# Optimization experiments

Hardware: AMD Instinct MI355X
Metric: run time of the kernel (lower is better)

Reference implementation:

```python
import jax, jax.numpy as jnp
import numpy as np

B, K, NP = 2, 48, 25            # batch, context_length, grid_x*grid_y
C, H, L = 768, 12, 6            # n_embd, n_head, n_layer
COLORS, VOCAB, IS = 10, 40, 26  # color_num, vocab_size, intention_size
MAXT = 1000                     # max_timestep
TOK = NP + 4                    # tokens per timestep (rtg, 25 states, action, pnp, intention)
T = K * TOK                     # total sequence length


def layernorm(x, g, b, eps=1e-5):
    m = x.mean(-1, keepdims=True)
    v = ((x - m) ** 2).mean(-1, keepdims=True)
    return (x - m) * jax.lax.rsqrt(v + eps) * g + b


def causal_attn(x, wq, bq, wk, bk, wv, bv, wo, bo):
    Bx, Tx, Cx = x.shape
    hd = Cx // H
    def heads(w, bb):
        return (x @ w + bb).reshape(Bx, Tx, H, hd).transpose(0, 2, 1, 3)
    q, k, v = heads(wq, bq), heads(wk, bk), heads(wv, bv)
    att = jnp.einsum('bhqd,bhkd->bhqk', q, k) * (1.0 / np.sqrt(hd))
    mask = jnp.tril(jnp.ones((Tx, Tx), bool))
    att = jnp.where(mask, att, -jnp.inf)
    att = jax.nn.softmax(att, axis=-1)
    y = jnp.einsum('bhqk,bhkd->bhqd', att, v).transpose(0, 2, 1, 3).reshape(Bx, Tx, Cx)
    return y @ wo + bo


def setup_inputs() -> dict:
    key = jax.random.key(0)
    ks = iter(jax.random.split(key, 64))
    def nrm(shape):
        return jax.random.normal(next(ks), shape, jnp.float32) * 0.02
    inp = dict(
        states=jax.random.randint(next(ks), (B, K * NP), 0, COLORS),
        actions=jax.random.randint(next(ks), (B, K), 0, VOCAB),
        rtgs=jax.random.normal(next(ks), (B, K), jnp.float32),
        timesteps=jax.random.randint(next(ks), (B, K), 0, MAXT + 1),
        pnp=jax.random.normal(next(ks), (B, K, NP), jnp.float32),
        intentions=jax.random.randint(next(ks), (B, K, 2), 0, IS),
        pos_emb=nrm((K + 1, C)),               # (block_size, C)
        global_pos_emb=nrm((MAXT + 1, C)),
        state_tab=nrm((COLORS, C)),
        action_tab=nrm((VOCAB, C)),
        ret_W=nrm((1, C)), ret_b=jnp.zeros((C,)),
        pnp_W=nrm((NP, C)), pnp_b=jnp.zeros((C,)),
        src_tab=nrm((IS, C)), dst_tab=nrm((IS, C)),
        int_W=nrm((2 * C, C)), int_b=jnp.zeros((C,)),
        ln1_g=jnp.ones((L, C)), ln1_b=jnp.zeros((L, C)),
        ln2_g=jnp.ones((L, C)), ln2_b=jnp.zeros((L, C)),
        Wq=nrm((L, C, C)), bq=jnp.zeros((L, C)),
        Wk=nrm((L, C, C)), bk=jnp.zeros((L, C)),
        Wv=nrm((L, C, C)), bv=jnp.zeros((L, C)),
        Wo=nrm((L, C, C)), bo=jnp.zeros((L, C)),
        Wm1=nrm((L, C, 4 * C)), bm1=jnp.zeros((L, 4 * C)),
        Wm2=nrm((L, 4 * C, C)), bm2=jnp.zeros((L, C)),
        lnf_g=jnp.ones((C,)), lnf_b=jnp.zeros((C,)),
        Whs=nrm((C, COLORS)), bhs=jnp.zeros((COLORS,)),
        Wha=nrm((C, VOCAB)), bha=jnp.zeros((VOCAB,)),
        Whr=nrm((C, 1)), bhr=jnp.zeros((1,)),
        Whi=nrm((C, 2 * IS)), bhi=jnp.zeros((2 * IS,)),
    )
    return inp


def reference(states, actions, rtgs, timesteps, pnp, intentions,
              pos_emb, global_pos_emb, state_tab, action_tab,
              ret_W, ret_b, pnp_W, pnp_b, src_tab, dst_tab, int_W, int_b,
              ln1_g, ln1_b, ln2_g, ln2_b, Wq, bq, Wk, bk, Wv, bv, Wo, bo,
              Wm1, bm1, Wm2, bm2, lnf_g, lnf_b,
              Whs, bhs, Wha, bha, Whr, bhr, Whi, bhi):
    # --- embeddings, interleaved as [rtg, state_0..24, action, pnp, intention] per timestep ---
    st = state_tab[states].reshape(B, K, NP, C)                    # strided writes 1+i::TOK
    ae = action_tab[actions][:, :, None, :]
    re = (rtgs[..., None] @ ret_W + ret_b)[:, :, None, :]          # rtgs.unsqueeze(-1) -> Linear(1,C)
    pe = (pnp @ pnp_W + pnp_b)[:, :, None, :]
    ie_in = jnp.concatenate([src_tab[intentions[..., 0]], dst_tab[intentions[..., 1]]], axis=-1)
    ie = (ie_in @ int_W + int_b)[:, :, None, :]
    tok = jnp.concatenate([re, st, ae, pe, ie], axis=2).reshape(B, T, C)
    # --- positions: gather global + local pos_emb[:block_size-1], repeat_interleave by TOK ---
    pos = global_pos_emb[timesteps] + pos_emb[:K][None]            # (B, K, C)
    x = tok + jnp.repeat(pos, TOK, axis=1)
    # --- transformer stack (dropout p=0) ---
    def blk(h, p):
        l1g, l1b, l2g, l2b, wq, bq_, wk, bk_, wv, bv_, wo, bo_, w1, b1, w2, b2 = p
        h = h + causal_attn(layernorm(h, l1g, l1b), wq, bq_, wk, bk_, wv, bv_, wo, bo_)
        m = layernorm(h, l2g, l2b)
        h = h + jax.nn.gelu(m @ w1 + b1, approximate=False) @ w2 + b2
        return h, None
    x, _ = jax.lax.scan(blk, x, (ln1_g, ln1_b, ln2_g, ln2_b, Wq, bq, Wk, bk, Wv, bv, Wo, bo, Wm1, bm1, Wm2, bm2))
    x = layernorm(x, lnf_g, lnf_b)
    xr = x.reshape(B, K, TOK, C)
    logits = x @ Whs + bhs                                         # (B, T, COLORS)
    logit_action = xr[:, :, NP + 1] @ Wha + bha                    # (B, K, VOCAB)
    logit_rtg = (xr[:, :, 0] @ Whr + bhr)[..., 0]                  # (B, K)
    li = xr[:, :, NP + 3] @ Whi + bhi                              # (B, K, 2*IS)
    return logits, logit_action, logit_rtg, li[..., :IS], li[..., IS:]
```

## Files before the change

kernel.cpp:

```cpp
#include <hip/hip_runtime.h>
#include <hip/hip_bf16.h>
#include <math.h>


typedef __hip_bfloat16 bf16;
typedef __attribute__((ext_vector_type(4))) short s4v;
typedef __attribute__((ext_vector_type(8))) short s8v;
typedef __attribute__((ext_vector_type(4))) float f4v;
typedef unsigned int u32;

#define DEV static __device__ __forceinline__

constexpr int NBATCH = 2;
constexpr int NK   = 48;
constexpr int NNP  = 25;
constexpr int NC   = 768;
constexpr int NH   = 12;
constexpr int NL   = 6;
constexpr int NTOK = 29;
constexpr int NT   = NK * NTOK;
constexpr int NM   = NBATCH * NT;
constexpr int MPAD = 2816;

DEV float bs2f(short s) {
  unsigned u = ((unsigned)(unsigned short)s) << 16;
  float f; __builtin_memcpy(&f, &u, 4); return f;
}
DEV short f2bs(float f) {
  bf16 h = __float2bfloat16(f);
  short s; __builtin_memcpy(&s, &h, 2); return s;
}

DEV void async16(const short* g, short* l) {
  __builtin_amdgcn_global_load_lds(
      (const __attribute__((address_space(1))) u32*)g,
      (__attribute__((address_space(3))) u32*)l, 16, 0, 0);
}

__global__ __launch_bounds__(256) void transpose_kernel(
    const float* __restrict__ src, bf16* __restrict__ dst, int R, int C)
{
  int c0 = blockIdx.x * 32, r0 = blockIdx.y * 32;
  __shared__ float tl[32][33];
  int rr = threadIdx.x >> 5, cc = threadIdx.x & 31;
#pragma unroll
  for (int p = 0; p < 4; p++)
    tl[rr + p * 8][cc] = src[(long)(r0 + rr + p * 8) * C + c0 + cc];
  __syncthreads();
#pragma unroll
  for (int p = 0; p < 4; p++)
    dst[(long)(c0 + rr + p * 8) * R + r0 + cc] = __float2bfloat16(tl[cc][rr + p * 8]);
}

__global__ __launch_bounds__(256) void transpose_layer_kernel(
    const float* __restrict__ Wq, const float* __restrict__ Wk,
    const float* __restrict__ Wv, const float* __restrict__ Wo,
    const float* __restrict__ Wm1, const float* __restrict__ Wm2,
    bf16* __restrict__ WqkvT, bf16* __restrict__ WoT,
    bf16* __restrict__ Wm1T, bf16* __restrict__ Wm2T, int multi)
{
  int blk = blockIdx.x;
  int l = blk / 1728, t = blk - l * 1728;
  long so = (long)l * 768 * 768;
  long mo = (long)l * 768 * 3072;
  long dl = multi ? l : 0;
  const float* src; bf16* dst; int R, C, tile;
  if (t < 432) {
    int m = t / 144; tile = t - m * 144;
    src = (m == 0 ? Wq : (m == 1 ? Wk : Wv)) + so;
    dst = WqkvT + dl * (2304L * 768) + (long)m * 768 * 768; R = 768; C = 768;
  } else if (t < 576)  { src = Wo + so;  dst = WoT  + dl * (768L * 768);  tile = t - 432;  R = 768;  C = 768;  }
  else if (t < 1152)   { src = Wm1 + mo; dst = Wm1T + dl * (3072L * 768); tile = t - 576;  R = 768;  C = 3072; }
  else                 { src = Wm2 + mo; dst = Wm2T + dl * (768L * 3072); tile = t - 1152; R = 3072; C = 768;  }
  int ct = C / 64;
  int tr = tile / ct, tc = tile - tr * ct;
  int r0 = tr * 64, c0 = tc * 64;

  __shared__ short tl[64][66];
  int t4 = threadIdx.x & 15, rr = threadIdx.x >> 4;
#pragma unroll
  for (int p = 0; p < 4; p++) {
    int row = rr + p * 16;
    f4v v = *(const f4v*)(src + (long)(r0 + row) * C + c0 + t4 * 4);
    tl[t4 * 4 + 0][row] = f2bs(v.x);
    tl[t4 * 4 + 1][row] = f2bs(v.y);
    tl[t4 * 4 + 2][row] = f2bs(v.z);
    tl[t4 * 4 + 3][row] = f2bs(v.w);
  }
  __syncthreads();
#pragma unroll
  for (int p = 0; p < 4; p++) {
    int drow = rr + p * 16;
    s4v w = *(const s4v*)&tl[drow][t4 * 4];
    *(s4v*)((short*)dst + (long)(c0 + drow) * R + r0 + t4 * 4) = w;
  }
}

__global__ __launch_bounds__(256) void gather_ie_kernel(
    const int* __restrict__ intentions, const float* __restrict__ src_tab,
    const float* __restrict__ dst_tab, bf16* __restrict__ ie_in)
{
  int idx = blockIdx.x * 256 + threadIdx.x;
  if (idx >= 96 * 1536) return;
  int row = idx / 1536, col = idx - row * 1536;
  float v;
  if (col < 768) v = src_tab[intentions[row * 2 + 0] * 768 + col];
  else           v = dst_tab[intentions[row * 2 + 1] * 768 + col - 768];
  ie_in[idx] = __float2bfloat16(v);
}

__global__ __launch_bounds__(256) void embed_kernel(
    const int* __restrict__ states, const int* __restrict__ actions,
    const float* __restrict__ rtgs, const int* __restrict__ timesteps,
    const float* __restrict__ pnp,
    const float* __restrict__ pos_emb, const float* __restrict__ gpe,
    const float* __restrict__ state_tab, const float* __restrict__ action_tab,
    const float* __restrict__ retW, const float* __restrict__ retb,
    const float* __restrict__ pnpW, const float* __restrict__ pnpb,
    const bf16* __restrict__ ieb, float* __restrict__ X)
{
  int bk = blockIdx.x;
  int b = bk / NK, ts = bk - b * NK;
  int c = blockIdx.y * 256 + threadIdx.x;

  float rtg = rtgs[bk];
  int tstep = timesteps[bk];
  int act   = actions[bk];

  long base = (long)(b * NT + ts * NTOK) * NC;
  float pos = gpe[(long)tstep * NC + c] + pos_emb[ts * NC + c];

  X[base + c] = rtg * retW[c] + retb[c] + pos;
  const int* sp = states + bk * NNP;
#pragma unroll
  for (int i = 0; i < NNP; i++)
    X[base + (1 + i) * NC + c] = state_tab[sp[i] * NC + c] + pos;
  X[base + 26 * NC + c] = action_tab[act * NC + c] + pos;
  float ap = pnpb[c];
  const float* pv = pnp + bk * NNP;
#pragma unroll
  for (int i = 0; i < NNP; i++) ap += pv[i] * pnpW[i * NC + c];
  X[base + 27 * NC + c] = ap + pos;
  X[base + 28 * NC + c] = __bfloat162float(ieb[bk * NC + c]) + pos;
}

__global__ __launch_bounds__(256) void ln_kernel(
    const float* __restrict__ X, bf16* __restrict__ XN,
    const float* __restrict__ g, const float* __restrict__ bt)
{
  int row = blockIdx.x, tid = threadIdx.x;
  const float* x = X + (long)row * NC;
  float v0 = x[tid], v1 = x[tid + 256], v2 = x[tid + 512];
  float s = v0 + v1 + v2;
#pragma unroll
  for (int o = 32; o > 0; o >>= 1) s += __shfl_down(s, o, 64);
  __shared__ float red[8];
  if ((tid & 63) == 0) red[tid >> 6] = s;
  __syncthreads();
  float mean = (red[0] + red[1] + red[2] + red[3]) * (1.0f / NC);
  float d0 = v0 - mean, d1 = v1 - mean, d2 = v2 - mean;
  float qq = d0 * d0 + d1 * d1 + d2 * d2;
#pragma unroll
  for (int o = 32; o > 0; o >>= 1) qq += __shfl_down(qq, o, 64);
  __syncthreads();
  if ((tid & 63) == 0) red[tid >> 6] = qq;
  __syncthreads();
  float var = (red[0] + red[1] + red[2] + red[3]) * (1.0f / NC);
  float rs = 1.0f / sqrtf(var + 1e-5f);
  bf16* xn = XN + (long)row * NC;
  xn[tid      ] = __float2bfloat16(d0 * rs * g[tid      ] + bt[tid      ]);
  xn[tid + 256] = __float2bfloat16(d1 * rs * g[tid + 256] + bt[tid + 256]);
  xn[tid + 512] = __float2bfloat16(d2 * rs * g[tid + 512] + bt[tid + 512]);
}

template<int BM, int BN>
__global__ __launch_bounds__(256) void gemm_kernel(
    const bf16* __restrict__ A, const bf16* __restrict__ WT,
    const float* __restrict__ b0, const float* __restrict__ b1,
    const float* __restrict__ b2, int Nsplit,
    bf16* __restrict__ outb, float* __restrict__ resid,
    int M, int N, int K, int flags)
{
  constexpr int IM  = BM / 64;
  constexpr int JN  = BN / 16;
  constexpr int ACH = BM / 64;
  constexpr int BCH = BN / 64;
  __shared__ __align__(1024) short As[2][BM * 32];
  __shared__ __align__(1024) short Bs[2][BN * 32];

  int tid = threadIdx.x, wave = tid >> 6, lane = tid & 63;
  int quad = lane >> 4, l16 = lane & 15;
  int m0 = blockIdx.y * BM, n0 = blockIdx.x * BN;
  int wm = wave * (BM / 4);
  int lr = lane >> 2, lc = (lane & 3) * 8;

  const short* Ag = (const short*)A + (long)m0 * K + lc;
  const short* Bg = (const short*)WT + (long)n0 * K + lc;

  const short* ag[ACH]; int alo[ACH];
#pragma unroll
  for (int c = 0; c < ACH; c++) {
    int rbase = wave * (16 * ACH) + c * 16;
    ag[c] = Ag + (long)(rbase + lr) * K;
    alo[c] = rbase * 32;
  }
  const short* bg[BCH]; int blo[BCH];
#pragma unroll
  for (int c = 0; c < BCH; c++) {
    int rbase = wave * (16 * BCH) + c * 16;
    bg[c] = Bg + (long)(rbase + lr) * K;
    blo[c] = rbase * 32;
  }

  f4v zero4 = {0.f, 0.f, 0.f, 0.f};
  f4v acc[IM][JN];
#pragma unroll
  for (int i = 0; i < IM; i++)
#pragma unroll
    for (int j = 0; j < JN; j++) acc[i][j] = zero4;

  int nk = K >> 5;
#pragma unroll
  for (int c = 0; c < ACH; c++) async16(ag[c], &As[0][alo[c]]);
#pragma unroll
  for (int c = 0; c < BCH; c++) async16(bg[c], &Bs[0][blo[c]]);
  __syncthreads();

  for (int kt = 0; kt < nk; kt++) {
    int cur = kt & 1, nxt = cur ^ 1;
    if (kt + 1 < nk) {
      int ko = (kt + 1) << 5;
#pragma unroll
      for (int c = 0; c < ACH; c++) async16(ag[c] + ko, &As[nxt][alo[c]]);
#pragma unroll
      for (int c = 0; c < BCH; c++) async16(bg[c] + ko, &Bs[nxt][blo[c]]);
    }
    s8v af[IM], bf8[JN];
#pragma unroll
    for (int i = 0; i < IM; i++) {
      const short* p = &As[cur][(wm + i * 16 + l16) * 32 + quad * 8];
      af[i].lo = *(const s4v*)p; af[i].hi = *(const s4v*)(p + 4);
    }
#pragma unroll
    for (int j = 0; j < JN; j++) {
      const short* p = &Bs[cur][(j * 16 + l16) * 32 + quad * 8];
      bf8[j].lo = *(const s4v*)p; bf8[j].hi = *(const s4v*)(p + 4);
    }
#pragma unroll
    for (int i = 0; i < IM; i++)
#pragma unroll
      for (int j = 0; j < JN; j++)
        acc[i][j] = __builtin_amdgcn_mfma_f32_16x16x32_bf16(af[i], bf8[j], acc[i][j], 0, 0, 0);
    __syncthreads();
  }

#pragma unroll
  for (int i = 0; i < IM; i++) {
    int rbase = m0 + wm + i * 16 + quad * 4;
#pragma unroll
    for (int j = 0; j < JN; j++) {
      int bc = n0 + j * 16;
      int wsel = bc / Nsplit;
      const float* bp = wsel == 0 ? b0 : (wsel == 1 ? b1 : b2);
      float bv = bp[bc - wsel * Nsplit + l16];
      int col = bc + l16;
#pragma unroll
      for (int r = 0; r < 4; r++) {
        int row = rbase + r;
        if (row < M) {
          float v = acc[i][j][r] + bv;
          if (flags & 1) v = 0.5f * v * (1.0f + erff(v * 0.70710678118654752f));
          if (flags & 2) resid[(long)row * N + col] += v;
          else outb[(long)row * N + col] = __float2bfloat16(v);
        }
      }
    }
  }
}

constexpr int ASTR = 72;

__global__ __launch_bounds__(256) void attn_kernel(
    const bf16* __restrict__ QKV, bf16* __restrict__ Yg)
{
  int qt = blockIdx.x, h = blockIdx.y, b = blockIdx.z;
  int q0 = qt * 64;
  int tid = threadIdx.x, wave = tid >> 6, lane = tid & 63, quad = lane >> 4, l16 = lane & 15;

  __shared__ short Qs[64 * ASTR];
  __shared__ short Ks[64 * ASTR];
  __shared__ short Vt[64 * ASTR];
  __shared__ short Ps[64 * ASTR];
  __shared__ float S[64 * 65];
  __shared__ float mrow[64], lrow[64], arow[64];
  __shared__ float red[256];

  if (tid < 64) { mrow[tid] = -1e30f; lrow[tid] = 0.f; }

  int r = tid >> 2, c16 = (tid & 3) * 16;
  const short* src = (const short*)QKV;
  s8v zz = {0,0,0,0,0,0,0,0};

  s8v qv0 = zz, qv1 = zz;
  if (q0 + r < NT) {
    const s8v* p = (const s8v*)(src + (long)(b * NT + q0 + r) * 2304 + h * 64 + c16);
    qv0 = p[0]; qv1 = p[1];
  }
  {
    short* qp = &Qs[r * ASTR + c16];
    *(s4v*)(qp    ) = qv0.lo; *(s4v*)(qp + 4) = qv0.hi;
    *(s4v*)(qp + 8) = qv1.lo; *(s4v*)(qp + 12) = qv1.hi;
  }

  f4v zero4 = {0.f, 0.f, 0.f, 0.f};
  f4v Of[4];
#pragma unroll
  for (int j = 0; j < 4; j++) Of[j] = zero4;

  int kend = q0 + 63; if (kend > NT - 1) kend = NT - 1;
  for (int k0 = 0; k0 <= kend; k0 += 64) {
    s8v kv0 = zz, kv1 = zz, vv0 = zz, vv1 = zz;
    if (k0 + r < NT) {
      const s8v* pk = (const s8v*)(src + (long)(b * NT + k0 + r) * 2304 + 768 + h * 64 + c16);
      kv0 = pk[0]; kv1 = pk[1];
      const s8v* pvv = (const s8v*)(src + (long)(b * NT + k0 + r) * 2304 + 1536 + h * 64 + c16);
      vv0 = pvv[0]; vv1 = pvv[1];
    }
    __syncthreads();
    {
      short* kp = &Ks[r * ASTR + c16];
      *(s4v*)(kp    ) = kv0.lo; *(s4v*)(kp + 4) = kv0.hi;
      *(s4v*)(kp + 8) = kv1.lo; *(s4v*)(kp + 12) = kv1.hi;
      short* vt = &Vt[c16 * ASTR + r];
      vt[ 0 * ASTR] = vv0.s0; vt[ 1 * ASTR] = vv0.s1; vt[ 2 * ASTR] = vv0.s2; vt[ 3 * ASTR] = vv0.s3;
      vt[ 4 * ASTR] = vv0.s4; vt[ 5 * ASTR] = vv0.s5; vt[ 6 * ASTR] = vv0.s6; vt[ 7 * ASTR] = vv0.s7;
      vt[ 8 * ASTR] = vv1.s0; vt[ 9 * ASTR] = vv1.s1; vt[10 * ASTR] = vv1.s2; vt[11 * ASTR] = vv1.s3;
      vt[12 * ASTR] = vv1.s4; vt[13 * ASTR] = vv1.s5; vt[14 * ASTR] = vv1.s6; vt[15 * ASTR] = vv1.s7;
    }
    __syncthreads();

    f4v sa[4];
#pragma unroll
    for (int j = 0; j < 4; j++) sa[j] = zero4;
#pragma unroll
    for (int ks = 0; ks < 2; ks++) {
      const short* pa = &Qs[(wave * 16 + l16) * ASTR + ks * 32 + quad * 8];
      s8v aq; aq.lo = *(const s4v*)pa; aq.hi = *(const s4v*)(pa + 4);
#pragma unroll
      for (int j = 0; j < 4; j++) {
        const short* pb = &Ks[(j * 16 + l16) * ASTR + ks * 32 + quad * 8];
        s8v bk8; bk8.lo = *(const s4v*)pb; bk8.hi = *(const s4v*)(pb + 4);
        sa[j] = __builtin_amdgcn_mfma_f32_16x16x32_bf16(aq, bk8, sa[j], 0, 0, 0);
      }
    }
#pragma unroll
    for (int j = 0; j < 4; j++) {
#pragma unroll
      for (int rg = 0; rg < 4; rg++) {
        int rloc = wave * 16 + quad * 4 + rg;
        int cloc = j * 16 + l16;
        int gq = q0 + rloc, gk = k0 + cloc;
        float sv = (gk <= gq && gq < NT) ? sa[j][rg] * 0.125f : -1e30f;
        S[rloc * 65 + cloc] = sv;
      }
    }
    __syncthreads();

    float mx = -1e30f;
#pragma unroll
    for (int c = 0; c < 16; c++) mx = fmaxf(mx, S[r * 65 + c16 + c]);
    red[r * 4 + (tid & 3)] = mx;
    __syncthreads();
    if (tid < 64) {
      float tm = fmaxf(fmaxf(red[tid * 4], red[tid * 4 + 1]), fmaxf(red[tid * 4 + 2], red[tid * 4 + 3]));
      float mn = fmaxf(mrow[tid], tm);
      arow[tid] = __expf(mrow[tid] - mn);
      mrow[tid] = mn;
    }
    __syncthreads();

    float mr = mrow[r];
    float psum = 0.f;
#pragma unroll
    for (int c = 0; c < 16; c++) {
      float e = __expf(S[r * 65 + c16 + c] - mr);
      psum += e;
      Ps[r * ASTR + c16 + c] = f2bs(e);
    }
    red[r * 4 + (tid & 3)] = psum;
    __syncthreads();
    if (tid < 64)
      lrow[tid] = lrow[tid] * arow[tid] + red[tid * 4] + red[tid * 4 + 1] + red[tid * 4 + 2] + red[tid * 4 + 3];
#pragma unroll
    for (int j = 0; j < 4; j++)
#pragma unroll
      for (int rg = 0; rg < 4; rg++)
        Of[j][rg] *= arow[wave * 16 + quad * 4 + rg];
    __syncthreads();

#pragma unroll
    for (int ks = 0; ks < 2; ks++) {
      const short* pa = &Ps[(wave * 16 + l16) * ASTR + ks * 32 + quad * 8];
      s8v ap8; ap8.lo = *(const s4v*)pa; ap8.hi = *(const s4v*)(pa + 4);
#pragma unroll
      for (int j = 0; j < 4; j++) {
        const short* pb = &Vt[(j * 16 + l16) * ASTR + ks * 32 + quad * 8];
        s8v vp8; vp8.lo = *(const s4v*)pb; vp8.hi = *(const s4v*)(pb + 4);
        Of[j] = __builtin_amdgcn_mfma_f32_16x16x32_bf16(ap8, vp8, Of[j], 0, 0, 0);
      }
    }
  }
  __syncthreads();
#pragma unroll
  for (int j = 0; j < 4; j++) {
#pragma unroll
    for (int rg = 0; rg < 4; rg++) {
      int rloc = wave * 16 + quad * 4 + rg;
      int gq = q0 + rloc;
      if (gq < NT) {
        float ov = Of[j][rg] / lrow[rloc];
        Yg[(long)(b * NT + gq) * NC + h * 64 + j * 16 + l16] = __float2bfloat16(ov);
      }
    }
  }
}

__global__ __launch_bounds__(256) void head_logits_kernel(
    const bf16* __restrict__ XN, const float* __restrict__ Whs,
    const float* __restrict__ bhs, float* __restrict__ out)
{
  int idx = blockIdx.x * 256 + threadIdx.x;
  if (idx >= NM * 10) return;
  int row = idx / 10, n = idx - row * 10;
  const short* x = (const short*)XN + (long)row * NC;
  float a0 = bhs[n], a1 = 0.f, a2 = 0.f, a3 = 0.f;
  for (int k = 0; k < NC; k += 4) {
    a0 += bs2f(x[k    ]) * Whs[(k    ) * 10 + n];
    a1 += bs2f(x[k + 1]) * Whs[(k + 1) * 10 + n];
    a2 += bs2f(x[k + 2]) * Whs[(k + 2) * 10 + n];
    a3 += bs2f(x[k + 3]) * Whs[(k + 3) * 10 + n];
  }
  out[idx] = a0 + a1 + a2 + a3;
}

__global__ __launch_bounds__(128) void head_small_kernel(
    const bf16* __restrict__ XN,
    const float* __restrict__ Wha, const float* __restrict__ bha,
    const float* __restrict__ Whr, const float* __restrict__ bhr,
    const float* __restrict__ Whi, const float* __restrict__ bhi,
    float* __restrict__ outA, float* __restrict__ outR,
    float* __restrict__ outS, float* __restrict__ outD)
{
  int blk = blockIdx.x;
  int b = blk / NK, ts = blk - b * NK;
  int tid = threadIdx.x;
  if (tid >= 93) return;
  const short* xs = (const short*)XN;
  if (tid < 40) {
    long row = (long)(b * NT + ts * NTOK + 26) * NC;
    float a0 = bha[tid], a1 = 0.f, a2 = 0.f, a3 = 0.f;
    for (int k = 0; k < NC; k += 4) {
      a0 += bs2f(xs[row + k    ]) * Wha[(k    ) * 40 + tid];
      a1 += bs2f(xs[row + k + 1]) * Wha[(k + 1) * 40 + tid];
      a2 += bs2f(xs[row + k + 2]) * Wha[(k + 2) * 40 + tid];
      a3 += bs2f(xs[row + k + 3]) * Wha[(k + 3) * 40 + tid];
    }
    outA[blk * 40 + tid] = a0 + a1 + a2 + a3;
  } else if (tid == 40) {
    long row = (long)(b * NT + ts * NTOK) * NC;
    float a0 = bhr[0], a1 = 0.f, a2 = 0.f, a3 = 0.f;
    for (int k = 0; k < NC; k += 4) {
      a0 += bs2f(xs[row + k    ]) * Whr[k    ];
      a1 += bs2f(xs[row + k + 1]) * Whr[k + 1];
      a2 += bs2f(xs[row + k + 2]) * Whr[k + 2];
      a3 += bs2f(xs[row + k + 3]) * Whr[k + 3];
    }
    outR[blk] = a0 + a1 + a2 + a3;
  } else {
    int n = tid - 41;
    long row = (long)(b * NT + ts * NTOK + 28) * NC;
    float a0 = bhi[n], a1 = 0.f, a2 = 0.f, a3 = 0.f;
    for (int k = 0; k < NC; k += 4) {
      a0 += bs2f(xs[row + k    ]) * Whi[(k    ) * 52 + n];
      a1 += bs2f(xs[row + k + 1]) * Whi[(k + 1) * 52 + n];
      a2 += bs2f(xs[row + k + 2]) * Whi[(k + 2) * 52 + n];
      a3 += bs2f(xs[row + k + 3]) * Whi[(k + 3) * 52 + n];
    }
    if (n < 26) outS[blk * 26 + n] = a0 + a1 + a2 + a3;
    else        outD[blk * 26 + (n - 26)] = a0 + a1 + a2 + a3;
  }
}

extern "C" void kernel_launch(void* const* d_in, const int* in_sizes, int n_in,
                              void* d_out, int out_size, void* d_ws, size_t ws_size,
                              hipStream_t stream)
{
  (void)in_sizes; (void)n_in; (void)out_size;

  const int*   states     = (const int*)  d_in[0];
  const int*   actions    = (const int*)  d_in[1];
  const float* rtgs       = (const float*)d_in[2];
  const int*   timesteps  = (const int*)  d_in[3];
  const float* pnp        = (const float*)d_in[4];
  const int*   intentions = (const int*)  d_in[5];
  const float* pos_emb    = (const float*)d_in[6];
  const float* gpe        = (const float*)d_in[7];
  const float* state_tab  = (const float*)d_in[8];
  const float* action_tab = (const float*)d_in[9];
  const float* retW  = (const float*)d_in[10];
  const float* retb  = (const float*)d_in[11];
  const float* pnpW  = (const float*)d_in[12];
  const float* pnpb  = (const float*)d_in[13];
  const float* src_tab = (const float*)d_in[14];
  const float* dst_tab = (const float*)d_in[15];
  const float* intW  = (const float*)d_in[16];
  const float* intb  = (const float*)d_in[17];
  const float* ln1g  = (const float*)d_in[18];
  const float* ln1b  = (const float*)d_in[19];
  const float* ln2g  = (const float*)d_in[20];
  const float* ln2b  = (const float*)d_in[21];
  const float* Wq = (const float*)d_in[22];
  const float* bq = (const float*)d_in[23];
  const float* Wk = (const float*)d_in[24];
  const float* bk = (const float*)d_in[25];
  const float* Wv = (const float*)d_in[26];
  const float* bv = (const float*)d_in[27];
  const float* Wo = (const float*)d_in[28];
  const float* bo = (const float*)d_in[29];
  const float* Wm1 = (const float*)d_in[30];
  const float* bm1 = (const float*)d_in[31];
  const float* Wm2 = (const float*)d_in[32];
  const float* bm2 = (const float*)d_in[33];
  const float* lnfg = (const float*)d_in[34];
  const float* lnfb = (const float*)d_in[35];
  const float* Whs = (const float*)d_in[36];
  const float* bhs = (const float*)d_in[37];
  const float* Wha = (const float*)d_in[38];
  const float* bha = (const float*)d_in[39];
  const float* Whr = (const float*)d_in[40];
  const float* bhr = (const float*)d_in[41];
  const float* Whi = (const float*)d_in[42];
  const float* bhi = (const float*)d_in[43];

  char* wsb = (char*)d_ws;
  float* X   = (float*)(wsb);
  bf16* XN   = (bf16*)(wsb + 8650752);
  bf16* QKVb = (bf16*)(wsb + 12976128);
  bf16* Yb   = (bf16*)(wsb + 25952256);
  bf16* H1   = QKVb;
  bf16* WTbase = (bf16*)(wsb + 30277632);

  const size_t NEED_BIG = 30277632UL + 84934656UL + 2949120UL;
  bool big = ws_size >= NEED_BIG;

  long sQKV = 2304L * 768, sO = 768L * 768, sM1 = 3072L * 768, sM2 = 768L * 3072;
  bf16 *WqkvT, *WoT, *Wm1T, *Wm2T, *intWT;
  if (big) {
    WqkvT = WTbase;
    WoT   = WqkvT + 6 * sQKV;
    Wm1T  = WoT   + 6 * sO;
    Wm2T  = Wm1T  + 6 * sM1;
    intWT = Wm2T  + 6 * sM2;
  } else {
    WqkvT = WTbase;
    WoT   = WqkvT + sQKV;
    Wm1T  = WoT + sO;
    Wm2T  = Wm1T + sM1;
    intWT = WTbase;
  }
  bf16* ie_in = intWT + 768L * 1536;
  bf16* ieb   = ie_in + 128L * 1536;

  float* out0 = (float*)d_out;
  float* out1 = out0 + 27840;
  float* out2 = out1 + 3840;
  float* out3 = out2 + 96;
  float* out4 = out3 + 2496;

  transpose_kernel<<<dim3(24, 48), 256, 0, stream>>>(intW, intWT, 1536, 768);
  gather_ie_kernel<<<(96 * 1536 + 255) / 256, 256, 0, stream>>>(intentions, src_tab, dst_tab, ie_in);
  gemm_kernel<64, 64><<<dim3(12, 2), 256, 0, stream>>>(ie_in, intWT, intb, intb, intb, 768,
      ieb, nullptr, 96, 768, 1536, 0);
  embed_kernel<<<dim3(96, 3), 256, 0, stream>>>(
      states, actions, rtgs, timesteps, pnp, pos_emb, gpe, state_tab, action_tab,
      retW, retb, pnpW, pnpb, ieb, X);

  if (big)
    transpose_layer_kernel<<<1728 * NL, 256, 0, stream>>>(
        Wq, Wk, Wv, Wo, Wm1, Wm2, WqkvT, WoT, Wm1T, Wm2T, 1);

  for (int l = 0; l < NL; l++) {
    const long wofs = (long)l * NC * NC;
    const long mofs = (long)l * NC * 4 * NC;
    if (!big)
      transpose_layer_kernel<<<1728, 256, 0, stream>>>(
          Wq + wofs, Wk + wofs, Wv + wofs, Wo + wofs, Wm1 + mofs, Wm2 + mofs,
          WqkvT, WoT, Wm1T, Wm2T, 0);
    bf16* wqkv = big ? WqkvT + l * sQKV : WqkvT;
    bf16* wo   = big ? WoT   + l * sO   : WoT;
    bf16* wm1  = big ? Wm1T  + l * sM1  : Wm1T;
    bf16* wm2  = big ? Wm2T  + l * sM2  : Wm2T;

    ln_kernel<<<NM, 256, 0, stream>>>(X, XN, ln1g + l * NC, ln1b + l * NC);
    gemm_kernel<128, 128><<<dim3(18, 22), 256, 0, stream>>>(XN, wqkv,
        bq + l * NC, bk + l * NC, bv + l * NC, 768, QKVb, nullptr, NM, 2304, NC, 0);
    attn_kernel<<<dim3(22, NH, NBATCH), 256, 0, stream>>>(QKVb, Yb);
    gemm_kernel<64, 64><<<dim3(12, 44), 256, 0, stream>>>(Yb, wo,
        bo + l * NC, bo + l * NC, bo + l * NC, 768, nullptr, X, NM, 768, NC, 2);
    ln_kernel<<<NM, 256, 0, stream>>>(X, XN, ln2g + l * NC, ln2b + l * NC);
    gemm_kernel<128, 128><<<dim3(24, 22), 256, 0, stream>>>(XN, wm1,
        bm1 + l * 4 * NC, bm1 + l * 4 * NC, bm1 + l * 4 * NC, 4 * NC, H1, nullptr,
        NM, 3072, NC, 1);
    gemm_kernel<64, 64><<<dim3(12, 44), 256, 0, stream>>>(H1, wm2,
        bm2 + l * NC, bm2 + l * NC, bm2 + l * NC, 768, nullptr, X, NM, 768, 4 * NC, 2);
  }
  ln_kernel<<<NM, 256, 0, stream>>>(X, XN, lnfg, lnfb);
  head_logits_kernel<<<(NM * 10 + 255) / 256, 256, 0, stream>>>(XN, Whs, bhs, out0);
  head_small_kernel<<<NBATCH * NK, 128, 0, stream>>>(XN, Wha, bha, Whr, bhr, Whi, bhi,
      out1, out2, out3, out4);
}
```

Baseline: 1.680 ms.

## Keep attention softmax in registers, prefetch next K/V tile, and shrink QKV/MLP1 GEMM tiles

The attention kernel now does the online softmax in registers with wave shuffles instead of a shared-memory score matrix and several block barriers. It also loads the next K/V tile into registers while the current tile is computed. Separately, the QKV and MLP-up GEMMs switch from 128x128 to 128x64 tiles, doubling the grid to fill more compute units. The register softmax adds register pressure, and the smaller tiles reduce data reuse per block.

Measured after the change: 1.624 ms. 3.3% less time.

```diff
diff --git a/kernel.cpp b/kernel.cpp
--- a/kernel.cpp
+++ b/kernel.cpp
@@ -291,11 +291,6 @@
   __shared__ short Ks[64 * ASTR];
   __shared__ short Vt[64 * ASTR];
   __shared__ short Ps[64 * ASTR];
-  __shared__ float S[64 * 65];
-  __shared__ float mrow[64], lrow[64], arow[64];
-  __shared__ float red[256];
-
-  if (tid < 64) { mrow[tid] = -1e30f; lrow[tid] = 0.f; }
 
   int r = tid >> 2, c16 = (tid & 3) * 16;
   const short* src = (const short*)QKV;
@@ -316,16 +311,21 @@
   f4v Of[4];
 #pragma unroll
   for (int j = 0; j < 4; j++) Of[j] = zero4;
+  float m_r[4], l_r[4];
+#pragma unroll
+  for (int rg = 0; rg < 4; rg++) { m_r[rg] = -1e30f; l_r[rg] = 0.f; }
 
   int kend = q0 + 63; if (kend > NT - 1) kend = NT - 1;
+
+  s8v kv0 = zz, kv1 = zz, vv0 = zz, vv1 = zz;
+  if (r < NT) {
+    const s8v* pk = (const s8v*)(src + (long)(b * NT + r) * 2304 + 768 + h * 64 + c16);
+    kv0 = pk[0]; kv1 = pk[1];
+    const s8v* pvv = (const s8v*)(src + (long)(b * NT + r) * 2304 + 1536 + h * 64 + c16);
+    vv0 = pvv[0]; vv1 = pvv[1];
+  }
+
   for (int k0 = 0; k0 <= kend; k0 += 64) {
-    s8v kv0 = zz, kv1 = zz, vv0 = zz, vv1 = zz;
-    if (k0 + r < NT) {
-      const s8v* pk = (const s8v*)(src + (long)(b * NT + k0 + r) * 2304 + 768 + h * 64 + c16);
-      kv0 = pk[0]; kv1 = pk[1];
-      const s8v* pvv = (const s8v*)(src + (long)(b * NT + k0 + r) * 2304 + 1536 + h * 64 + c16);
-      vv0 = pvv[0]; vv1 = pvv[1];
-    }
     __syncthreads();
     {
       short* kp = &Ks[r * ASTR + c16];
@@ -339,6 +339,15 @@
     }
     __syncthreads();
 
+    int k1 = k0 + 64;
+    s8v nk0 = zz, nk1 = zz, nv0 = zz, nv1 = zz;
+    if (k1 <= kend && k1 + r < NT) {
+      const s8v* pk = (const s8v*)(src + (long)(b * NT + k1 + r) * 2304 + 768 + h * 64 + c16);
+      nk0 = pk[0]; nk1 = pk[1];
+      const s8v* pvv = (const s8v*)(src + (long)(b * NT + k1 + r) * 2304 + 1536 + h * 64 + c16);
+      nv0 = pvv[0]; nv1 = pvv[1];
+    }
+
     f4v sa[4];
 #pragma unroll
     for (int j = 0; j < 4; j++) sa[j] = zero4;
@@ -353,49 +362,48 @@
         sa[j] = __builtin_amdgcn_mfma_f32_16x16x32_bf16(aq, bk8, sa[j], 0, 0, 0);
       }
     }
+
 #pragma unroll
     for (int j = 0; j < 4; j++) {
 #pragma unroll
       for (int rg = 0; rg < 4; rg++) {
-        int rloc = wave * 16 + quad * 4 + rg;
-        int cloc = j * 16 + l16;
-        int gq = q0 + rloc, gk = k0 + cloc;
-        float sv = (gk <= gq && gq < NT) ? sa[j][rg] * 0.125f : -1e30f;
-        S[rloc * 65 + cloc] = sv;
+        int gq = q0 + wave * 16 + quad * 4 + rg;
+        int gk = k0 + j * 16 + l16;
+        sa[j][rg] = (gk <= gq && gq < NT) ? sa[j][rg] * 0.125f : -1e30f;
       }
     }
-    __syncthreads();
-
-    float mx = -1e30f;
-#pragma unroll
-    for (int c = 0; c < 16; c++) mx = fmaxf(mx, S[r * 65 + c16 + c]);
-    red[r * 4 + (tid & 3)] = mx;
-    __syncthreads();
-    if (tid < 64) {
-      float tm = fmaxf(fmaxf(red[tid * 4], red[tid * 4 + 1]), fmaxf(red[tid * 4 + 2], red[tid * 4 + 3]));
-      float mn = fmaxf(mrow[tid], tm);
-      arow[tid] = __expf(mrow[tid] - mn);
-      mrow[tid] = mn;
-    }
-    __syncthreads();
-
-    float mr = mrow[r];
-    float psum = 0.f;
-#pragma unroll
-    for (int c = 0; c < 16; c++) {
-      float e = __expf(S[r * 65 + c16 + c] - mr);
-      psum += e;
-      Ps[r * ASTR + c16 + c] = f2bs(e);
-    }
-    red[r * 4 + (tid & 3)] = psum;
-    __syncthreads();
-    if (tid < 64)
-      lrow[tid] = lrow[tid] * arow[tid] + red[tid * 4] + red[tid * 4 + 1] + red[tid * 4 + 2] + red[tid * 4 + 3];
+
+#pragma unroll
+    for (int rg = 0; rg < 4; rg++) {
+      float mx = fmaxf(fmaxf(sa[0][rg], sa[1][rg]), fmaxf(sa[2][rg], sa[3][rg]));
+      mx = fmaxf(mx, __shfl_xor(mx, 1));
+      mx = fmaxf(mx, __shfl_xor(mx, 2));
+      mx = fmaxf(mx, __shfl_xor(mx, 4));
+      mx = fmaxf(mx, __shfl_xor(mx, 8));
+      float mn = fmaxf(m_r[rg], mx);
+      float al = __expf(m_r[rg] - mn);
+      m_r[rg] = mn;
+      float ps = 0.f;
+#pragma unroll
+      for (int j = 0; j < 4; j++) {
+        float e = __expf(sa[j][rg] - mn);
+        sa[j][rg] = e;
+        ps += e;
+      }
+      ps += __shfl_xor(ps, 1);
+      ps += __shfl_xor(ps, 2);
+      ps += __shfl_xor(ps, 4);
+      ps += __shfl_xor(ps, 8);
+      l_r[rg] = l_r[rg] * al + ps;
+#pragma unroll
+      for (int j = 0; j < 4; j++) Of[j][rg] *= al;
+    }
+
 #pragma unroll
     for (int j = 0; j < 4; j++)
 #pragma unroll
       for (int rg = 0; rg < 4; rg++)
-        Of[j][rg] *= arow[wave * 16 + quad * 4 + rg];
+        Ps[(wave * 16 + quad * 4 + rg) * ASTR + j * 16 + l16] = f2bs(sa[j][rg]);
     __syncthreads();
 
 #pragma unroll
@@ -409,16 +417,19 @@
         Of[j] = __builtin_amdgcn_mfma_f32_16x16x32_bf16(ap8, vp8, Of[j], 0, 0, 0);
       }
     }
-  }
-  __syncthreads();
-#pragma unroll
-  for (int j = 0; j < 4; j++) {
-#pragma unroll
-    for (int rg = 0; rg < 4; rg++) {
-      int rloc = wave * 16 + quad * 4 + rg;
-      int gq = q0 + rloc;
-      if (gq < NT) {
-        float ov = Of[j][rg] / lrow[rloc];
+
+    kv0 = nk0; kv1 = nk1; vv0 = nv0; vv1 = nv1;
+  }
+
+#pragma unroll
+  for (int rg = 0; rg < 4; rg++) {
+    int rloc = wave * 16 + quad * 4 + rg;
+    int gq = q0 + rloc;
+    if (gq < NT) {
+      float inv = 1.0f / l_r[rg];
+#pragma unroll
+      for (int j = 0; j < 4; j++) {
+        float ov = Of[j][rg] * inv;
         Yg[(long)(b * NT + gq) * NC + h * 64 + j * 16 + l16] = __float2bfloat16(ov);
       }
     }
@@ -602,13 +613,13 @@
     bf16* wm2  = big ? Wm2T  + l * sM2  : Wm2T;
 
     ln_kernel<<<NM, 256, 0, stream>>>(X, XN, ln1g + l * NC, ln1b + l * NC);
-    gemm_kernel<128, 128><<<dim3(18, 22), 256, 0, stream>>>(XN, wqkv,
+    gemm_kernel<128, 64><<<dim3(36, 22), 256, 0, stream>>>(XN, wqkv,
         bq + l * NC, bk + l * NC, bv + l * NC, 768, QKVb, nullptr, NM, 2304, NC, 0);
     attn_kernel<<<dim3(22, NH, NBATCH), 256, 0, stream>>>(QKVb, Yb);
     gemm_kernel<64, 64><<<dim3(12, 44), 256, 0, stream>>>(Yb, wo,
         bo + l * NC, bo + l * NC, bo + l * NC, 768, nullptr, X, NM, 768, NC, 2);
     ln_kernel<<<NM, 256, 0, stream>>>(X, XN, ln2g + l * NC, ln2b + l * NC);
-    gemm_kernel<128, 128><<<dim3(24, 22), 256, 0, stream>>>(XN, wm1,
+    gemm_kernel<128, 64><<<dim3(48, 22), 256, 0, stream>>>(XN, wm1,
         bm1 + l * 4 * NC, bm1 + l * 4 * NC, bm1 + l * 4 * NC, 4 * NC, H1, nullptr,
         NM, 3072, NC, 1);
     gemm_kernel<64, 64><<<dim3(12, 44), 256, 0, stream>>>(H1, wm2,
```
